# Performance work log

Hardware: AMD Instinct MI355X
Metric: run time of the kernel (lower is better)

Reference implementation:

```python
import math
import jax, jax.numpy as jnp
import numpy as np

D_MODEL = 1024
N_HEAD = 16
HEAD_DIM = D_MODEL // N_HEAD
MAX_LENGTH = 2048


def sinusoid_table():
    # Matches RelativeEmbedding.get_embedding with num_embeddings = max_length + 1
    num_emb = MAX_LENGTH + 1
    half = HEAD_DIM // 2
    freq = jnp.exp(jnp.arange(half, dtype=jnp.float32) * (-math.log(10000.0) / (half - 1)))
    lo = -((num_emb + 1) // 2)  # python floor of -num_emb//2
    hi = num_emb // 2
    pos = jnp.arange(lo, hi, dtype=jnp.float32)  # length num_emb
    ang = pos[:, None] * freq[None, :]
    table = jnp.concatenate([jnp.sin(ang), jnp.cos(ang)], axis=1)  # (num_emb, HEAD_DIM)
    origin_shift = num_emb // 2 + 1
    return table, origin_shift


def _shift(BD):
    # (b, n, L, 2L) -> (b, n, L, L) diagonal-shift trick
    b, n, L, _ = BD.shape
    BD = jnp.concatenate([BD, jnp.zeros((b, n, L, 1), BD.dtype)], axis=-1)
    BD = BD.reshape(b, n, -1, L)[:, :, :-1, :].reshape(b, n, L, -1)
    return BD[:, :, :, :L]


def setup_inputs() -> dict:
    key = jax.random.key(0)
    k1, k2, k3, k4 = jax.random.split(key, 4)
    B, L = 2, 1024
    x = jax.random.normal(k1, (B, L, D_MODEL), dtype=jnp.float32)
    mask = jnp.ones((B, L), dtype=jnp.int32)
    W_qv = jax.random.normal(k2, (2 * D_MODEL, D_MODEL), dtype=jnp.float32) * 0.02
    r_r_bias = jax.random.normal(k3, (N_HEAD, HEAD_DIM), dtype=jnp.float32) * 0.02
    r_w_bias = jax.random.normal(k4, (N_HEAD, HEAD_DIM), dtype=jnp.float32) * 0.02
    return {"x": x, "mask": mask, "W_qv": W_qv, "r_r_bias": r_r_bias, "r_w_bias": r_w_bias}


def reference(x, mask, W_qv, r_r_bias, r_w_bias):
    B, L, d = x.shape
    table, origin_shift = sinusoid_table()
    pos = jnp.arange(-L, L) + origin_shift
    pos_embed = table[pos]  # (2L, head_dim)

    qv = x @ W_qv.T  # (B, L, 2d)
    q, v = jnp.split(qv, 2, axis=-1)
    q = q.reshape(B, L, N_HEAD, HEAD_DIM).transpose(0, 2, 1, 3)  # (B,H,L,dh)
    k = x.reshape(B, L, N_HEAD, HEAD_DIM).transpose(0, 2, 1, 3)
    v = v.reshape(B, L, N_HEAD, HEAD_DIM).transpose(0, 2, 1, 3)

    AC = jnp.einsum('bnqd,bnkd->bnqk', q + r_r_bias[None, :, None, :], k)
    D_ = jnp.einsum('nd,ld->nl', r_w_bias, pos_embed)[None, :, None, :]  # (1,H,1,2L)
    B_ = jnp.einsum('bnqd,ld->bnql', q, pos_embed)  # (B,H,L,2L)
    BD = _shift(B_ + D_)

    attn = AC + BD
    attn = jnp.where(mask[:, None, None, :] == 0, -jnp.inf, attn)
    attn = jax.nn.softmax(attn, axis=-1)
    out = jnp.einsum('bnqk,bnkd->bnqd', attn, v)
    return out.transpose(0, 2, 1, 3).reshape(B, L, d)
```

## Files before the change

### kernel.cpp

```cpp
#include <hip/hip_runtime.h>
#include <hip/hip_bf16.h>
#include <math.h>

#define L_SEQ 1024
#define TWO_L 2048
#define NHEAD 16
#define HD 64
#define DM 1024
#define BATCH 2
#define PE2R 2176
#define GBS 132

typedef _Float16 f16;
typedef _Float16 f16x4 __attribute__((ext_vector_type(4)));
typedef _Float16 f16x8 __attribute__((ext_vector_type(8)));
typedef float f32x4 __attribute__((ext_vector_type(4)));

__device__ __forceinline__ f16x8 ld8(const f16* p) {
  f16x4 lo = *(const f16x4*)p;
  f16x4 hi = *(const f16x4*)(p + 16);
  f16x8 r;
  r[0] = lo[0]; r[1] = lo[1]; r[2] = lo[2]; r[3] = lo[3];
  r[4] = hi[0]; r[5] = hi[1]; r[6] = hi[2]; r[7] = hi[3];
  return r;
}

__device__ __forceinline__ float pe_val(int j, int d) {
  float posval = (float)(j - L_SEQ);
  float freq = expf(-(float)(d & 31) * 0.2971077539347156f);
  float ang = posval * freq;
  return (d < 32) ? sinf(ang) : cosf(ang);
}

__global__ __launch_bounds__(256) void prep1(const float* __restrict__ x,
                                             const float* __restrict__ W,
                                             f16* __restrict__ pe2,
                                             f16* __restrict__ xh,
                                             f16* __restrict__ Wh) {
  int bid = blockIdx.x, tid = threadIdx.x;
  if (bid < 2048) {
    int i = (bid * 256 + tid) * 4;
    float4 v = *(const float4*)(x + i);
    f16x4 o = {(f16)v.x, (f16)v.y, (f16)v.z, (f16)v.w};
    *(f16x4*)(xh + i) = o;
  } else if (bid < 4096) {
    int i = ((bid - 2048) * 256 + tid) * 4;
    float4 v = *(const float4*)(W + i);
    f16x4 o = {(f16)v.x, (f16)v.y, (f16)v.z, (f16)v.w};
    *(f16x4*)(Wh + i) = o;
  } else {
    int idx = (bid - 4096) * 256 + tid;
    int rrow = idx >> 6, d = idx & 63;
    int u = rrow - 1088;
    int j = (u < 0) ? u + 2049 : u;
    float v = (j != 2048) ? pe_val(j, d) : 0.f;
    pe2[idx] = (f16)v;
  }
}

__global__ __launch_bounds__(256) void prep2(const float* __restrict__ rr,
                                             const float* __restrict__ rw,
                                             const f16* __restrict__ pe2,
                                             float* __restrict__ D2x) {
  int idx = blockIdx.x * 256 + threadIdx.x;
  int h = idx / PE2R, r0 = idx - h * PE2R;
  float s = 0.f;
#pragma unroll
  for (int d = 0; d < HD; ++d)
    s = fmaf(rw[h * HD + d] - rr[h * HD + d], (float)pe2[r0 * HD + d], s);
  D2x[idx] = s;
}

#define QV_STEP(T, AS, BS, CA0, CA1, CB0, CB1, NA0, NA1, NB0, NB1)             \
  {                                                                            \
    *(f16x8*)&AS[r * 72 + c] = CA0;                                            \
    *(f16x8*)&AS[r * 72 + c + 8] = CA1;                                        \
    *(f16x8*)&BS[r * 72 + c] = CB0;                                            \
    *(f16x8*)&BS[r * 72 + c + 8] = CB1;                                        \
    __syncthreads();                                                           \
    if ((T) + 1 < 16) {                                                        \
      const f16* na = ga + ((T) + 1) * 64;                                     \
      NA0 = *(const f16x8*)na;                                                 \
      NA1 = *(const f16x8*)(na + 8);                                           \
      const f16* nb = gb + ((T) + 1) * 64;                                     \
      NB0 = *(const f16x8*)nb;                                                 \
      NB1 = *(const f16x8*)(nb + 8);                                           \
    }                                                                          \
    _Pragma("unroll")                                                          \
    for (int kc = 0; kc < 2; ++kc) {                                           \
      f16x8 a = ld8(&AS[(w * 16 + li) * 72 + kc * 32 + g * 4]);                \
      _Pragma("unroll")                                                        \
      for (int nf = 0; nf < 4; ++nf) {                                         \
        f16x8 bfr = ld8(&BS[(nf * 16 + li) * 72 + kc * 32 + g * 4]);           \
        s[nf] = __builtin_amdgcn_mfma_f32_16x16x32_f16(a, bfr, s[nf], 0, 0, 0);\
      }                                                                        \
    }                                                                          \
  }

__global__ __launch_bounds__(256) void qv_mfma(const f16* __restrict__ xh,
                                               const f16* __restrict__ Wh,
                                               f16* __restrict__ qvh,
                                               f16* __restrict__ vT) {
  __shared__ f16 As0[64 * 72], As1[64 * 72];
  __shared__ f16 Bs0[64 * 72], Bs1[64 * 72];
  int tid = threadIdx.x;
  int w = tid >> 6, lane = tid & 63, g = lane >> 4, li = lane & 15;
  int m0 = blockIdx.y * 64, n0 = blockIdx.x * 64;
  int r = tid >> 2, c = (tid & 3) * 16;

  const f16* ga = xh + (size_t)(m0 + r) * 1024 + c;
  const f16* gb = Wh + (size_t)(n0 + r) * 1024 + c;
  f16x8 ca0 = *(const f16x8*)ga, ca1 = *(const f16x8*)(ga + 8);
  f16x8 cb0 = *(const f16x8*)gb, cb1 = *(const f16x8*)(gb + 8);
  f16x8 na0, na1, nb0, nb1;

  f32x4 s[4];
#pragma unroll
  for (int i = 0; i < 4; ++i) s[i] = {0.f, 0.f, 0.f, 0.f};

  for (int t = 0; t < 16; t += 2) {
    QV_STEP(t, As0, Bs0, ca0, ca1, cb0, cb1, na0, na1, nb0, nb1);
    QV_STEP(t + 1, As1, Bs1, na0, na1, nb0, nb1, ca0, ca1, cb0, cb1);
  }

#pragma unroll
  for (int nf = 0; nf < 4; ++nf) {
    int n = n0 + nf * 16 + li;
#pragma unroll
    for (int rr2 = 0; rr2 < 4; ++rr2) {
      int m = m0 + w * 16 + g * 4 + rr2;
      f16 val = (f16)s[nf][rr2];
      if (n < 1024) {
        qvh[(size_t)m * 2048 + n] = val;
      } else {
        int b_ = m >> 10, ls = m & 1023, hd = n - 1024;
        vT[((size_t)(b_ * 16 + (hd >> 6)) * 64 + (hd & 63)) * 1024 + ls] = val;
      }
    }
  }
}

#define BANDFILL(TT, QOFF, PEREG, D2V)                                         \
  {                                                                            \
    _Pragma("unroll")                                                          \
    for (int qf = 0; qf < 4; ++qf) {                                           \
      f32x4 gacc = {0.f, 0.f, 0.f, 0.f};                                       \
      _Pragma("unroll")                                                        \
      for (int kc = 0; kc < 2; ++kc) {                                         \
        f16x8 qo = ld8(&Qs[((QOFF) + qf * 16 + li) * 72 + kc * 32 + g * 4]);   \
        gacc = __builtin_amdgcn_mfma_f32_16x16x32_f16(PEREG[kc], qo, gacc, 0, 0, 0); \
      }                                                                        \
      f16x4 gpk;                                                               \
      gpk[0] = (f16)(gacc[0] + (D2V).x); gpk[1] = (f16)(gacc[1] + (D2V).y);    \
      gpk[2] = (f16)(gacc[2] + (D2V).z); gpk[3] = (f16)(gacc[3] + (D2V).w);    \
      *(f16x4*)&Gb[(qf * 16 + li) * GBS + (TT) + w * 16 + g * 4] = gpk;        \
    }                                                                          \
  }

#define ATTN_STEP(T, CK0, CK1, CV0, CV1, NK0, NK1, NV0, NV1, CPE, NPE)         \
  {                                                                            \
    const int k0 = (T) * 64;                                                   \
    const int tt = (64 * (T)) & 127;                                           \
    const int qoff = (64 * (T) >= q0) ? 1 : 0;                                 \
    *(f16x8*)&Ks[r * 72 + c] = CK0;                                            \
    *(f16x8*)&Ks[r * 72 + c + 8] = CK1;                                        \
    *(f16x8*)&Vs[r * 72 + c] = CV0;                                            \
    *(f16x8*)&Vs[r * 72 + c + 8] = CV1;                                        \
    float4 d2v = *(const float4*)(D2x + hD2 + 1088 + k0 - q0 + w * 16 + g * 4);\
    BANDFILL(tt, qoff, CPE, d2v)                                               \
    __syncthreads();                                                           \
    if ((T) + 1 < 16) {                                                        \
      const f16* nk = gk + (size_t)((T) + 1) * 64 * 1024;                      \
      NK0 = *(const f16x8*)nk;                                                 \
      NK1 = *(const f16x8*)(nk + 8);                                           \
      const f16* nv = gv + ((T) + 1) * 64;                                     \
      NV0 = *(const f16x8*)nv;                                                 \
      NV1 = *(const f16x8*)(nv + 8);                                           \
      const f16* pb = pe2 + (size_t)(1088 + 64 * ((T) + 1) - q0 + w * 16 + li) * 64; \
      NPE[0] = ld8(pb + g * 4);                                                \
      NPE[1] = ld8(pb + 32 + g * 4);                                           \
    }                                                                          \
    float gf[16];                                                              \
    {                                                                          \
      const int cb0 = tt + g * 4 - qi + 128;                                   \
      _Pragma("unroll")                                                        \
      for (int kf = 0; kf < 4; ++kf)                                           \
        _Pragma("unroll")                                                      \
        for (int u2 = 0; u2 < 4; ++u2)                                         \
          gf[kf * 4 + u2] = (float)Gb[qi * GBS + ((cb0 + kf * 16 + u2) & 127)];\
    }                                                                          \
    f32x4 s[4];                                                                \
    _Pragma("unroll")                                                          \
    for (int i = 0; i < 4; ++i) s[i] = {0.f, 0.f, 0.f, 0.f};                   \
    __builtin_amdgcn_s_setprio(1);                                             \
    _Pragma("unroll")                                                          \
    for (int kc = 0; kc < 2; ++kc) {                                           \
      f16x8 qb = ld8(&Qs[(1 + w * 16 + li) * 72 + kc * 32 + g * 4]);           \
      _Pragma("unroll")                                                        \
      for (int kf = 0; kf < 4; ++kf) {                                         \
        f16x8 ka = ld8(&Ks[(kf * 16 + li) * 72 + kc * 32 + g * 4]);            \
        s[kf] = __builtin_amdgcn_mfma_f32_16x16x32_f16(ka, qb, s[kf], 0, 0, 0);\
      }                                                                        \
    }                                                                          \
    __builtin_amdgcn_s_setprio(0);                                             \
    float sv[16];                                                              \
    float tmax = -1e30f;                                                       \
    _Pragma("unroll")                                                          \
    for (int kf = 0; kf < 4; ++kf) {                                           \
      _Pragma("unroll")                                                        \
      for (int rr2 = 0; rr2 < 4; ++rr2) {                                      \
        float v_ = s[kf][rr2] + gf[kf * 4 + rr2] +                             \
                   Ms[k0 + kf * 16 + g * 4 + rr2];                             \
        sv[kf * 4 + rr2] = v_;                                                 \
        tmax = fmaxf(tmax, v_);                                                \
      }                                                                        \
    }                                                                          \
    tmax = fmaxf(tmax, __shfl_xor(tmax, 16));                                  \
    tmax = fmaxf(tmax, __shfl_xor(tmax, 32));                                  \
    if (!__all(tmax <= m_run + 8.f)) {                                         \
      float mnew = fmaxf(m_run, tmax);                                         \
      float scale = __expf(m_run - mnew);                                      \
      m_run = mnew;                                                            \
      l_run *= scale;                                                          \
      _Pragma("unroll")                                                        \
      for (int f = 0; f < 4; ++f) {                                            \
        o[f][0] *= scale; o[f][1] *= scale; o[f][2] *= scale; o[f][3] *= scale;\
      }                                                                        \
    }                                                                          \
    float pf[16];                                                              \
    float lloc = 0.f;                                                          \
    _Pragma("unroll")                                                          \
    for (int i = 0; i < 16; ++i) { pf[i] = __expf(sv[i] - m_run); lloc += pf[i]; } \
    l_run += lloc;                                                             \
    f16x8 pb0, pb1;                                                            \
    _Pragma("unroll")                                                          \
    for (int i = 0; i < 8; ++i) { pb0[i] = (f16)pf[i]; pb1[i] = (f16)pf[8 + i]; } \
    __builtin_amdgcn_s_setprio(1);                                             \
    _Pragma("unroll")                                                          \
    for (int f = 0; f < 4; ++f) {                                              \
      f16x8 va0 = ld8(&Vs[(f * 16 + li) * 72 + g * 4]);                        \
      o[f] = __builtin_amdgcn_mfma_f32_16x16x32_f16(va0, pb0, o[f], 0, 0, 0);  \
      f16x8 va1 = ld8(&Vs[(f * 16 + li) * 72 + 32 + g * 4]);                   \
      o[f] = __builtin_amdgcn_mfma_f32_16x16x32_f16(va1, pb1, o[f], 0, 0, 0);  \
    }                                                                          \
    __builtin_amdgcn_s_setprio(0);                                             \
    __syncthreads();                                                           \
  }

__global__ __launch_bounds__(256) void attn_mfma(const f16* __restrict__ xh,
                                                 const f16* __restrict__ qvh,
                                                 const f16* __restrict__ vT,
                                                 const f16* __restrict__ pe2,
                                                 const float* __restrict__ D2x,
                                                 const int* __restrict__ mask,
                                                 const float* __restrict__ rr,
                                                 float* __restrict__ out) {
  __shared__ f16 Qs[65 * 72];
  __shared__ f16 Ks[64 * 72], Vs[64 * 72];
  __shared__ f16 Gb[64 * GBS];
  __shared__ float Ms[L_SEQ];
  int tid = threadIdx.x;
  int w = tid >> 6, lane = tid & 63, g = lane >> 4, li = lane & 15;
  int bid = blockIdx.x;
  int swz = (bid & 7) * 64 + (bid >> 3);
  int q0 = (swz & 15) * 64;
  int bh = swz >> 4;
  int b = bh >> 4, h = bh & 15;
  int r = tid >> 2, c = (tid & 3) * 16;
  const int qi = w * 16 + li;
  const int hD2 = h * PE2R;

#pragma unroll
  for (int i = 0; i < 4; ++i) {
    int k = tid + i * 256;
    Ms[k] = mask[b * L_SEQ + k] ? 0.f : -1e30f;
  }
  {
    int gq = q0 - 1 + r;
    if (gq < 0) gq = 0;
    const f16* src = qvh + (size_t)(b * L_SEQ + gq) * 2048 + h * HD + c;
#pragma unroll
    for (int u = 0; u < 16; ++u)
      Qs[r * 72 + c + u] = (f16)((float)src[u] + rr[h * HD + c + u]);
    if (tid < 4) {
      int c2 = tid * 16;
      const f16* s2 = qvh + (size_t)(b * L_SEQ + q0 + 63) * 2048 + h * HD + c2;
#pragma unroll
      for (int u = 0; u < 16; ++u)
        Qs[64 * 72 + c2 + u] = (f16)((float)s2[u] + rr[h * HD + c2 + u]);
    }
  }

  const f16* gk = xh + (size_t)(b * L_SEQ + r) * 1024 + h * HD + c;
  const f16* gv = vT + ((size_t)bh * 64 + r) * 1024 + c;
  f16x8 cka = *(const f16x8*)gk, ckb = *(const f16x8*)(gk + 8);
  f16x8 cva = *(const f16x8*)gv, cvb = *(const f16x8*)(gv + 8);
  f16x8 nka, nkb, nva, nvb;
  f16x8 peP[2], peA[2], peB[2];
  {
    const f16* pp = pe2 + (size_t)(1024 - q0 + w * 16 + li) * 64;
    peP[0] = ld8(pp + g * 4);
    peP[1] = ld8(pp + 32 + g * 4);
    const f16* p0 = pe2 + (size_t)(1088 - q0 + w * 16 + li) * 64;
    peA[0] = ld8(p0 + g * 4);
    peA[1] = ld8(p0 + 32 + g * 4);
  }

  __syncthreads();

  {
    float4 d2p = *(const float4*)(D2x + hD2 + 1024 - q0 + w * 16 + g * 4);
    BANDFILL(64, 0, peP, d2p)
  }

  float m_run = -1e30f, l_run = 0.f;
  f32x4 o[4];
#pragma unroll
  for (int i = 0; i < 4; ++i) o[i] = {0.f, 0.f, 0.f, 0.f};

  for (int t = 0; t < 16; t += 2) {
    ATTN_STEP(t, cka, ckb, cva, cvb, nka, nkb, nva, nvb, peA, peB);
    ATTN_STEP(t + 1, nka, nkb, nva, nvb, cka, ckb, cva, cvb, peB, peA);
  }

  float lt = l_run;
  lt += __shfl_xor(lt, 16);
  lt += __shfl_xor(lt, 32);
  float inv = 1.0f / lt;
  int qrow = q0 + qi;
  float* op = out + ((size_t)(b * L_SEQ + qrow)) * DM + h * HD;
#pragma unroll
  for (int f = 0; f < 4; ++f) {
    float4 res = {o[f][0] * inv, o[f][1] * inv, o[f][2] * inv, o[f][3] * inv};
    *(float4*)(op + f * 16 + g * 4) = res;
  }
}

extern "C" void kernel_launch(void* const* d_in, const int* in_sizes, int n_in,
                              void* d_out, int out_size, void* d_ws, size_t ws_size,
                              hipStream_t stream) {
  const float* x = (const float*)d_in[0];
  const int* mask = (const int*)d_in[1];
  const float* W = (const float*)d_in[2];
  const float* rr = (const float*)d_in[3];
  const float* rw = (const float*)d_in[4];
  float* out = (float*)d_out;

  f16* pe2 = (f16*)d_ws;
  float* D2x = (float*)(pe2 + (size_t)PE2R * 64);
  f16* xh = (f16*)(D2x + 16 * PE2R);
  f16* Wh = xh + 2097152;
  f16* qvh = Wh + 2097152;
  f16* vT = qvh + 4194304;

  prep1<<<4096 + (PE2R * 64) / 256, 256, 0, stream>>>(x, W, pe2, xh, Wh);
  prep2<<<(16 * PE2R) / 256, 256, 0, stream>>>(rr, rw, pe2, D2x);
  qv_mfma<<<dim3(32, 32), 256, 0, stream>>>(xh, Wh, qvh, vT);
  attn_mfma<<<512, 256, 0, stream>>>(xh, qvh, vT, pe2, D2x, mask, rr, out);
}
```

Baseline: 91.87 us.

## Split attention over two key halves with a combine pass; fold prep2 into qv kernel

The attention kernel now splits the key range into two halves, so the grid goes from 512 to 1024 blocks. Each block writes unnormalized partial outputs plus its running max and sum, and a new combine kernel merges the two halves with softmax rescaling. The D2x precompute moves into extra blocks of the qv GEMM launch, which removes one kernel launch. This is meant to raise occupancy on a GPU with many CUs, at the cost of extra global traffic for the partials and one more launch.

```diff
diff --git a/kernel.cpp b/kernel.cpp
--- a/kernel.cpp
+++ b/kernel.cpp
@@ -58,19 +58,6 @@
   }
 }
 
-__global__ __launch_bounds__(256) void prep2(const float* __restrict__ rr,
-                                             const float* __restrict__ rw,
-                                             const f16* __restrict__ pe2,
-                                             float* __restrict__ D2x) {
-  int idx = blockIdx.x * 256 + threadIdx.x;
-  int h = idx / PE2R, r0 = idx - h * PE2R;
-  float s = 0.f;
-#pragma unroll
-  for (int d = 0; d < HD; ++d)
-    s = fmaf(rw[h * HD + d] - rr[h * HD + d], (float)pe2[r0 * HD + d], s);
-  D2x[idx] = s;
-}
-
 #define QV_STEP(T, AS, BS, CA0, CA1, CB0, CB1, NA0, NA1, NB0, NB1)             \
   {                                                                            \
     *(f16x8*)&AS[r * 72 + c] = CA0;                                            \
@@ -100,12 +87,29 @@
 __global__ __launch_bounds__(256) void qv_mfma(const f16* __restrict__ xh,
                                                const f16* __restrict__ Wh,
                                                f16* __restrict__ qvh,
-                                               f16* __restrict__ vT) {
+                                               f16* __restrict__ vT,
+                                               const float* __restrict__ rr,
+                                               const float* __restrict__ rw,
+                                               const f16* __restrict__ pe2,
+                                               float* __restrict__ D2x) {
   __shared__ f16 As0[64 * 72], As1[64 * 72];
   __shared__ f16 Bs0[64 * 72], Bs1[64 * 72];
   int tid = threadIdx.x;
+  int bid = blockIdx.x;
+  if (bid >= 1024) {
+    int idx = (bid - 1024) * 256 + tid;
+    if (idx < 16 * PE2R) {
+      int h = idx / PE2R, r0 = idx - h * PE2R;
+      float s = 0.f;
+#pragma unroll
+      for (int d = 0; d < HD; ++d)
+        s = fmaf(rw[h * HD + d] - rr[h * HD + d], (float)pe2[r0 * HD + d], s);
+      D2x[idx] = s;
+    }
+    return;
+  }
   int w = tid >> 6, lane = tid & 63, g = lane >> 4, li = lane & 15;
-  int m0 = blockIdx.y * 64, n0 = blockIdx.x * 64;
+  int m0 = (bid >> 5) * 64, n0 = (bid & 31) * 64;
   int r = tid >> 2, c = (tid & 3) * 16;
 
   const f16* ga = xh + (size_t)(m0 + r) * 1024 + c;
@@ -169,7 +173,7 @@
     float4 d2v = *(const float4*)(D2x + hD2 + 1088 + k0 - q0 + w * 16 + g * 4);\
     BANDFILL(tt, qoff, CPE, d2v)                                               \
     __syncthreads();                                                           \
-    if ((T) + 1 < 16) {                                                        \
+    if ((T) + 1 < tend) {                                                      \
       const f16* nk = gk + (size_t)((T) + 1) * 64 * 1024;                      \
       NK0 = *(const f16x8*)nk;                                                 \
       NK1 = *(const f16x8*)(nk + 8);                                           \
@@ -254,7 +258,8 @@
                                                  const float* __restrict__ D2x,
                                                  const int* __restrict__ mask,
                                                  const float* __restrict__ rr,
-                                                 float* __restrict__ out) {
+                                                 float* __restrict__ opart,
+                                                 float* __restrict__ mlbuf) {
   __shared__ f16 Qs[65 * 72];
   __shared__ f16 Ks[64 * 72], Vs[64 * 72];
   __shared__ f16 Gb[64 * GBS];
@@ -262,13 +267,16 @@
   int tid = threadIdx.x;
   int w = tid >> 6, lane = tid & 63, g = lane >> 4, li = lane & 15;
   int bid = blockIdx.x;
-  int swz = (bid & 7) * 64 + (bid >> 3);
+  int bid9 = bid & 511;
+  int kh = bid >> 9;
+  int swz = (bid9 & 7) * 64 + (bid9 >> 3);
   int q0 = (swz & 15) * 64;
   int bh = swz >> 4;
   int b = bh >> 4, h = bh & 15;
   int r = tid >> 2, c = (tid & 3) * 16;
   const int qi = w * 16 + li;
   const int hD2 = h * PE2R;
+  const int t0 = kh * 8, tend = t0 + 8;
 
 #pragma unroll
   for (int i = 0; i < 4; ++i) {
@@ -293,15 +301,17 @@
 
   const f16* gk = xh + (size_t)(b * L_SEQ + r) * 1024 + h * HD + c;
   const f16* gv = vT + ((size_t)bh * 64 + r) * 1024 + c;
-  f16x8 cka = *(const f16x8*)gk, ckb = *(const f16x8*)(gk + 8);
-  f16x8 cva = *(const f16x8*)gv, cvb = *(const f16x8*)(gv + 8);
+  f16x8 cka = *(const f16x8*)(gk + (size_t)t0 * 64 * 1024);
+  f16x8 ckb = *(const f16x8*)(gk + (size_t)t0 * 64 * 1024 + 8);
+  f16x8 cva = *(const f16x8*)(gv + t0 * 64);
+  f16x8 cvb = *(const f16x8*)(gv + t0 * 64 + 8);
   f16x8 nka, nkb, nva, nvb;
   f16x8 peP[2], peA[2], peB[2];
   {
-    const f16* pp = pe2 + (size_t)(1024 - q0 + w * 16 + li) * 64;
+    const f16* pp = pe2 + (size_t)(1024 + 64 * t0 - q0 + w * 16 + li) * 64;
     peP[0] = ld8(pp + g * 4);
     peP[1] = ld8(pp + 32 + g * 4);
-    const f16* p0 = pe2 + (size_t)(1088 - q0 + w * 16 + li) * 64;
+    const f16* p0 = pe2 + (size_t)(1088 + 64 * t0 - q0 + w * 16 + li) * 64;
     peA[0] = ld8(p0 + g * 4);
     peA[1] = ld8(p0 + 32 + g * 4);
   }
@@ -309,8 +319,9 @@
   __syncthreads();
 
   {
-    float4 d2p = *(const float4*)(D2x + hD2 + 1024 - q0 + w * 16 + g * 4);
-    BANDFILL(64, 0, peP, d2p)
+    const int qoffP = (64 * (t0 - 1) >= q0) ? 1 : 0;
+    float4 d2p = *(const float4*)(D2x + hD2 + 1024 + 64 * t0 - q0 + w * 16 + g * 4);
+    BANDFILL(64, qoffP, peP, d2p)
   }
 
   float m_run = -1e30f, l_run = 0.f;
@@ -318,7 +329,7 @@
 #pragma unroll
   for (int i = 0; i < 4; ++i) o[i] = {0.f, 0.f, 0.f, 0.f};
 
-  for (int t = 0; t < 16; t += 2) {
+  for (int t = t0; t < tend; t += 2) {
     ATTN_STEP(t, cka, ckb, cva, cvb, nka, nkb, nva, nvb, peA, peB);
     ATTN_STEP(t + 1, nka, nkb, nva, nvb, cka, ckb, cva, cvb, peB, peA);
   }
@@ -326,14 +337,39 @@
   float lt = l_run;
   lt += __shfl_xor(lt, 16);
   lt += __shfl_xor(lt, 32);
-  float inv = 1.0f / lt;
   int qrow = q0 + qi;
-  float* op = out + ((size_t)(b * L_SEQ + qrow)) * DM + h * HD;
+  size_t prow = (size_t)(kh * 32 + bh) * L_SEQ + qrow;
+  float* op = opart + prow * 64;
 #pragma unroll
   for (int f = 0; f < 4; ++f) {
-    float4 res = {o[f][0] * inv, o[f][1] * inv, o[f][2] * inv, o[f][3] * inv};
+    float4 res = {o[f][0], o[f][1], o[f][2], o[f][3]};
     *(float4*)(op + f * 16 + g * 4) = res;
   }
+  if (g == 0) {
+    mlbuf[prow * 2] = m_run;
+    mlbuf[prow * 2 + 1] = lt;
+  }
+}
+
+__global__ __launch_bounds__(256) void combine(const float* __restrict__ opart,
+                                               const float* __restrict__ mlbuf,
+                                               float* __restrict__ out) {
+  int gid = blockIdx.x * 256 + threadIdx.x;
+  int e = gid * 4;
+  int qh = e >> 6;
+  int d0 = e & 63;
+  float m0v = mlbuf[(size_t)qh * 2], l0v = mlbuf[(size_t)qh * 2 + 1];
+  float m1v = mlbuf[(size_t)(32768 + qh) * 2], l1v = mlbuf[(size_t)(32768 + qh) * 2 + 1];
+  float4 o0 = *(const float4*)(opart + (size_t)qh * 64 + d0);
+  float4 o1 = *(const float4*)(opart + (size_t)(32768 + qh) * 64 + d0);
+  float M = fmaxf(m0v, m1v);
+  float w0 = __expf(m0v - M), w1 = __expf(m1v - M);
+  float inv = 1.0f / (l0v * w0 + l1v * w1);
+  int bh = qh >> 10, q = qh & 1023;
+  int b = bh >> 4, h = bh & 15;
+  float4 res = {(o0.x * w0 + o1.x * w1) * inv, (o0.y * w0 + o1.y * w1) * inv,
+                (o0.z * w0 + o1.z * w1) * inv, (o0.w * w0 + o1.w * w1) * inv};
+  *(float4*)(out + (size_t)(b * L_SEQ + q) * DM + h * HD + d0) = res;
 }
 
 extern "C" void kernel_launch(void* const* d_in, const int* in_sizes, int n_in,
@@ -352,9 +388,11 @@
   f16* Wh = xh + 2097152;
   f16* qvh = Wh + 2097152;
   f16* vT = qvh + 4194304;
+  float* opart = (float*)(vT + 2097152);
+  float* mlbuf = opart + 4194304;
 
   prep1<<<4096 + (PE2R * 64) / 256, 256, 0, stream>>>(x, W, pe2, xh, Wh);
-  prep2<<<(16 * PE2R) / 256, 256, 0, stream>>>(rr, rw, pe2, D2x);
-  qv_mfma<<<dim3(32, 32), 256, 0, stream>>>(xh, Wh, qvh, vT);
-  attn_mfma<<<512, 256, 0, stream>>>(xh, qvh, vT, pe2, D2x, mask, rr, out);
-}
+  qv_mfma<<<1024 + (16 * PE2R + 255) / 256, 256, 0, stream>>>(xh, Wh, qvh, vT, rr, rw, pe2, D2x);
+  attn_mfma<<<1024, 256, 0, stream>>>(xh, qvh, vT, pe2, D2x, mask, rr, opart, mlbuf);
+  combine<<<2048, 256, 0, stream>>>(opart, mlbuf, out);
+}
```

Result: slower. 97.90 us (+6.6%).
